# Optimization experiments

Hardware: AMD Instinct MI355X
Metric: run time of the kernel (lower is better)

The kernel has to match this reference:

```python
import jax, jax.numpy as jnp
import numpy as np

POS_LEN = 32  # S = POS_LEN**2 = 1024
NUM_F = 16    # fourier features -> input dim 8*16 = 128
HIDDEN = 256
T = 32        # gab_num_templates


def _offsets(pos_len):
    S = pos_len * pos_len
    s_idx = jnp.arange(S)
    s_r = s_idx // pos_len
    s_c = s_idx % pos_len
    dr = (s_r[:, None] - s_r[None, :]).astype(jnp.float32)
    dc = (s_c[:, None] - s_c[None, :]).astype(jnp.float32)
    return dr, dc


def setup_inputs() -> dict:
    key = jax.random.key(0)
    k1, k2, k3, k4 = jax.random.split(key, 4)
    # learnable freqs: exp(linspace(log(1), log(1/50)))
    freqs = jnp.exp(jnp.linspace(jnp.log(1.0), jnp.log(1.0 / 50.0), NUM_F)).astype(jnp.float32)
    fin = 8 * NUM_F
    W1 = jax.random.normal(k1, (HIDDEN, fin), dtype=jnp.float32) * (1.0 / np.sqrt(fin))
    b1 = jax.random.normal(k2, (HIDDEN,), dtype=jnp.float32) * 0.01
    W2 = jax.random.normal(k3, (T, HIDDEN), dtype=jnp.float32) * (1.0 / np.sqrt(HIDDEN))
    b2 = jax.random.normal(k4, (T,), dtype=jnp.float32) * 0.01
    dr, dc = _offsets(POS_LEN)
    return {"seq_len": POS_LEN * POS_LEN, "freqs": freqs, "W1": W1, "b1": b1,
            "W2": W2, "b2": b2, "dr": dr, "dc": dc}


def _fourier_features(dr, dc, freqs):
    # dr, dc: (S, S); freqs: (F,) -> (S, S, 8F)
    f = freqs[None, None, :]
    a = dr[..., None] * f
    b = dc[..., None] * f
    p = (dr + dc)[..., None] * f
    m = (dr - dc)[..., None] * f
    return jnp.concatenate([jnp.sin(a), jnp.cos(a), jnp.sin(b), jnp.cos(b),
                            jnp.sin(p), jnp.cos(p), jnp.sin(m), jnp.cos(m)], axis=-1)


def reference(seq_len, freqs, W1, b1, W2, b2, dr, dc):
    dr_s = dr[:seq_len, :seq_len]
    dc_s = dc[:seq_len, :seq_len]
    feats = _fourier_features(dr_s, dc_s, freqs)          # (S, S, 8F)
    h = jax.nn.silu(jnp.einsum('ijf,hf->ijh', feats, W1) + b1)  # (S, S, H)
    out = jnp.einsum('ijh,th->ijt', h, W2) + b2            # (S, S, T)
    return out * (1.0 / jnp.sqrt(jnp.float32(T)))
```

## Files before the change

kernel.cpp:

```cpp
#include <hip/hip_runtime.h>
#include <math.h>

#define NUM_F   16
#define FIN     (8 * NUM_F)
#define HIDDEN  256
#define TOUT    32
#define NOFF    63
#define NSUM    125
#define NPAIRS_TBL (NOFF * NOFF)
#define PROWS   (NOFF + NOFF + NSUM + NSUM)

typedef float vfloat4 __attribute__((ext_vector_type(4)));

__global__ __launch_bounds__(256) void gab_ptab_kernel(
    const float* __restrict__ freqs, const float* __restrict__ W1,
    float* __restrict__ P)
{
    __shared__ float fv[32];
    const int rho = blockIdx.x;
    int grp, val;
    if (rho < NOFF)                 { grp = 0; val = rho - 31; }
    else if (rho < 2 * NOFF)        { grp = 1; val = rho - NOFF - 31; }
    else if (rho < 2 * NOFF + NSUM) { grp = 2; val = rho - 2 * NOFF - 62; }
    else                            { grp = 3; val = rho - 2 * NOFF - NSUM - 62; }
    const int t = threadIdx.x;
    if (t < 32) {
        const float arg = (float)val * freqs[t & 15];
        fv[t] = (t < 16) ? sinf(arg) : cosf(arg);
    }
    __syncthreads();
    const float4* __restrict__ w4 = (const float4*)(W1 + t * FIN + grp * 32);
    const float4* f4 = (const float4*)fv;
    float a0 = 0.f, a1 = 0.f, a2 = 0.f, a3 = 0.f;
    #pragma unroll
    for (int k = 0; k < 8; k += 2) {
        const float4 wa = w4[k], wb = w4[k + 1];
        const float4 fa = f4[k], fb = f4[k + 1];
        a0 = fmaf(wa.x, fa.x, a0); a1 = fmaf(wa.y, fa.y, a1);
        a2 = fmaf(wa.z, fa.z, a2); a3 = fmaf(wa.w, fa.w, a3);
        a0 = fmaf(wb.x, fb.x, a0); a1 = fmaf(wb.y, fb.y, a1);
        a2 = fmaf(wb.z, fb.z, a2); a3 = fmaf(wb.w, fb.w, a3);
    }
    P[rho * HIDDEN + t] = (a0 + a1) + (a2 + a3);
}

__global__ __launch_bounds__(256) void gab_table_kernel(
    const float* __restrict__ P, const float* __restrict__ b1,
    const float* __restrict__ W2, const float* __restrict__ b2,
    float* __restrict__ table)
{
    const int pair = blockIdx.x * 4 + (threadIdx.x >> 6);
    if (pair >= NPAIRS_TBL) return;
    const int l = threadIdx.x & 63;
    const int ia = pair / NOFF;
    const int ib = pair % NOFF;
    const int ip = ia + ib;
    const int im = ia - ib + 62;
    const float4* __restrict__ P4 = (const float4*)P;
    const float4 pa = P4[(0 * NOFF          + ia) * 64 + l];
    const float4 pb = P4[(1 * NOFF          + ib) * 64 + l];
    const float4 pp = P4[(2 * NOFF          + ip) * 64 + l];
    const float4 pm = P4[((2 * NOFF + NSUM) + im) * 64 + l];
    const float4 bb = ((const float4*)b1)[l];
    float h0 = pa.x + pb.x + pp.x + pm.x + bb.x;
    float h1 = pa.y + pb.y + pp.y + pm.y + bb.y;
    float h2 = pa.z + pb.z + pp.z + pm.z + bb.z;
    float h3 = pa.w + pb.w + pp.w + pm.w + bb.w;
    h0 = h0 / (1.0f + expf(-h0));
    h1 = h1 / (1.0f + expf(-h1));
    h2 = h2 / (1.0f + expf(-h2));
    h3 = h3 / (1.0f + expf(-h3));
    float acc[32];
    const float4* __restrict__ W24 = (const float4*)W2;
    #pragma unroll
    for (int o = 0; o < 32; ++o) {
        const float4 w = W24[o * 64 + l];
        acc[o] = fmaf(w.x, h0, fmaf(w.y, h1, fmaf(w.z, h2, w.w * h3)));
    }
    #pragma unroll
    for (int i = 0; i < 16; ++i) {
        const float keep = (l & 1) ? acc[i + 16] : acc[i];
        const float send = (l & 1) ? acc[i] : acc[i + 16];
        acc[i] = keep + __shfl_xor(send, 1);
    }
    #pragma unroll
    for (int i = 0; i < 8; ++i) {
        const float keep = (l & 2) ? acc[i + 8] : acc[i];
        const float send = (l & 2) ? acc[i] : acc[i + 8];
        acc[i] = keep + __shfl_xor(send, 2);
    }
    #pragma unroll
    for (int i = 0; i < 4; ++i) {
        const float keep = (l & 4) ? acc[i + 4] : acc[i];
        const float send = (l & 4) ? acc[i] : acc[i + 4];
        acc[i] = keep + __shfl_xor(send, 4);
    }
    #pragma unroll
    for (int i = 0; i < 2; ++i) {
        const float keep = (l & 8) ? acc[i + 2] : acc[i];
        const float send = (l & 8) ? acc[i] : acc[i + 2];
        acc[i] = keep + __shfl_xor(send, 8);
    }
    {
        const float keep = (l & 16) ? acc[1] : acc[0];
        const float send = (l & 16) ? acc[0] : acc[1];
        acc[0] = keep + __shfl_xor(send, 16);
    }
    const float tot = acc[0] + __shfl_xor(acc[0], 32);
    if (l < 32) {
        const int o = ((l & 1) << 4) | ((l & 2) << 2) | (l & 4)
                    | ((l & 8) >> 2) | ((l & 16) >> 4);
        table[pair * TOUT + o] = (tot + b2[o]) * 0.17677669529663687f;
    }
}

__global__ __launch_bounds__(256) void gab_gather_kernel(
    const float* __restrict__ table,
    vfloat4* __restrict__ out, int npairs)
{
    const int total = npairs * 8;
    const int stride = gridDim.x * blockDim.x;
    const vfloat4* __restrict__ tbl4 = (const vfloat4*)table;
    for (int idx = blockIdx.x * blockDim.x + threadIdx.x; idx < total; idx += stride) {
        const int p = idx >> 3;
        const int l = idx & 7;
        const int i = p >> 10;
        const int j = p & 1023;
        const int ir = (i >> 5) - (j >> 5) + (NOFF / 2);
        const int ic = (i & 31) - (j & 31) + (NOFF / 2);
        const vfloat4 v = tbl4[(ir * NOFF + ic) * (TOUT / 4) + l];
        __builtin_nontemporal_store(v, &out[idx]);
    }
}

extern "C" void kernel_launch(void* const* d_in, const int* in_sizes, int n_in,
                              void* d_out, int out_size, void* d_ws, size_t ws_size,
                              hipStream_t stream) {
    const float* freqs = (const float*)d_in[1];
    const float* W1    = (const float*)d_in[2];
    const float* b1    = (const float*)d_in[3];
    const float* W2    = (const float*)d_in[4];
    const float* b2    = (const float*)d_in[5];
    vfloat4* out = (vfloat4*)d_out;

    const int npairs = in_sizes[6];

    const size_t TBL_B = (size_t)NPAIRS_TBL * TOUT * 4;
    float* table = (float*)d_ws;
    float* P     = (float*)((char*)d_ws + TBL_B);

    gab_ptab_kernel <<<PROWS, 256, 0, stream>>>(freqs, W1, P);
    gab_table_kernel<<<(NPAIRS_TBL + 3) / 4, 256, 0, stream>>>(P, b1, W2, b2, table);
    gab_gather_kernel<<<2048, 256, 0, stream>>>(table, out, npairs);
}
```

Measured before the change: 41.41 us.

## Fuse table build and gather into one scatter kernel writing output directly

```diff
diff --git a/kernel.cpp b/kernel.cpp
--- a/kernel.cpp
+++ b/kernel.cpp
@@ -9,8 +9,6 @@
 #define NSUM    125
 #define NPAIRS_TBL (NOFF * NOFF)
 #define PROWS   (NOFF + NOFF + NSUM + NSUM)
-
-typedef float vfloat4 __attribute__((ext_vector_type(4)));
 
 __global__ __launch_bounds__(256) void gab_ptab_kernel(
     const float* __restrict__ freqs, const float* __restrict__ W1,
@@ -44,18 +42,20 @@
     P[rho * HIDDEN + t] = (a0 + a1) + (a2 + a3);
 }
 
-__global__ __launch_bounds__(256) void gab_table_kernel(
+__global__ __launch_bounds__(256) void gab_scatter_kernel(
     const float* __restrict__ P, const float* __restrict__ b1,
     const float* __restrict__ W2, const float* __restrict__ b2,
-    float* __restrict__ table)
+    float* __restrict__ out)
 {
     const int pair = blockIdx.x * 4 + (threadIdx.x >> 6);
     if (pair >= NPAIRS_TBL) return;
     const int l = threadIdx.x & 63;
+
     const int ia = pair / NOFF;
     const int ib = pair % NOFF;
     const int ip = ia + ib;
     const int im = ia - ib + 62;
+
     const float4* __restrict__ P4 = (const float4*)P;
     const float4 pa = P4[(0 * NOFF          + ia) * 64 + l];
     const float4 pb = P4[(1 * NOFF          + ib) * 64 + l];
@@ -70,6 +70,7 @@
     h1 = h1 / (1.0f + expf(-h1));
     h2 = h2 / (1.0f + expf(-h2));
     h3 = h3 / (1.0f + expf(-h3));
+
     float acc[32];
     const float4* __restrict__ W24 = (const float4*)W2;
     #pragma unroll
@@ -107,29 +108,25 @@
         acc[0] = keep + __shfl_xor(send, 16);
     }
     const float tot = acc[0] + __shfl_xor(acc[0], 32);
-    if (l < 32) {
-        const int o = ((l & 1) << 4) | ((l & 2) << 2) | (l & 4)
-                    | ((l & 8) >> 2) | ((l & 16) >> 4);
-        table[pair * TOUT + o] = (tot + b2[o]) * 0.17677669529663687f;
-    }
-}
 
-__global__ __launch_bounds__(256) void gab_gather_kernel(
-    const float* __restrict__ table,
-    vfloat4* __restrict__ out, int npairs)
-{
-    const int total = npairs * 8;
-    const int stride = gridDim.x * blockDim.x;
-    const vfloat4* __restrict__ tbl4 = (const vfloat4*)table;
-    for (int idx = blockIdx.x * blockDim.x + threadIdx.x; idx < total; idx += stride) {
-        const int p = idx >> 3;
-        const int l = idx & 7;
-        const int i = p >> 10;
-        const int j = p & 1023;
-        const int ir = (i >> 5) - (j >> 5) + (NOFF / 2);
-        const int ic = (i & 31) - (j & 31) + (NOFF / 2);
-        const vfloat4 v = tbl4[(ir * NOFF + ic) * (TOUT / 4) + l];
-        __builtin_nontemporal_store(v, &out[idx]);
+    const int o = ((l & 1) << 4) | ((l & 2) << 2) | (l & 4)
+                | ((l & 8) >> 2) | ((l & 16) >> 4);
+    const float val = (tot + b2[o]) * 0.17677669529663687f;
+
+    const int dr = ia - 31, dc = ib - 31;
+    const int brmin = (dr > 0) ? dr : 0;
+    const int irmin = (dc > 0) ? dc : 0;
+    const int wc = 32 - ((dc < 0) ? -dc : dc);
+    const int hb = 32 - ((dr < 0) ? -dr : dr);
+    const int count = hb * wc;
+    const unsigned M = ((1u << 20) + (unsigned)wc - 1) / (unsigned)wc;
+
+    for (int m = (l >> 5); m < count; m += 2) {
+        const int q = (int)(((unsigned)m * M) >> 20);
+        const int r = m - q * wc;
+        const int i = ((brmin + q) << 5) + (irmin + r);
+        const int j = ((brmin + q - dr) << 5) + (irmin + r - dc);
+        __builtin_nontemporal_store(val, &out[(((i << 10) + j) << 5) + o]);
     }
 }
 
@@ -141,15 +138,10 @@
     const float* b1    = (const float*)d_in[3];
     const float* W2    = (const float*)d_in[4];
     const float* b2    = (const float*)d_in[5];
-    vfloat4* out = (vfloat4*)d_out;
+    float* out = (float*)d_out;
 
-    const int npairs = in_sizes[6];
+    float* P = (float*)d_ws;
 
-    const size_t TBL_B = (size_t)NPAIRS_TBL * TOUT * 4;
-    float* table = (float*)d_ws;
-    float* P     = (float*)((char*)d_ws + TBL_B);
-
-    gab_ptab_kernel <<<PROWS, 256, 0, stream>>>(freqs, W1, P);
-    gab_table_kernel<<<(NPAIRS_TBL + 3) / 4, 256, 0, stream>>>(P, b1, W2, b2, table);
-    gab_gather_kernel<<<2048, 256, 0, stream>>>(table, out, npairs);
+    gab_ptab_kernel   <<<PROWS, 256, 0, stream>>>(freqs, W1, P);
+    gab_scatter_kernel<<<(NPAIRS_TBL + 3) / 4, 256, 0, stream>>>(P, b1, W2, b2, out);
 }
```

After: 44.64 us. 1.08x slower.
